# Performance work log

Hardware: AMD Instinct MI355X
Metric: run time of the kernel (lower is better)

The kernel has to match this reference:

```python
import jax, jax.numpy as jnp
import numpy as np

N_NODES = 50000
N_EDGES = 600000
D_OBJ = 128
D_REL = 128
D_OUT = 128


def setup_inputs() -> dict:
    key = jax.random.key(0)
    ks = jax.random.split(key, 7)
    s_obj = 1.0 / np.sqrt(D_OBJ)
    s_rel = 1.0 / np.sqrt(D_REL)
    return {
        "obj_vecs": jax.random.normal(ks[0], (N_NODES, D_OBJ), dtype=jnp.float32),
        "rel_vecs": jax.random.normal(ks[1], (N_EDGES, D_REL), dtype=jnp.float32),
        "edge_index": jax.random.randint(ks[2], (N_EDGES, 2), 0, N_NODES, dtype=jnp.int64),
        "W_obj": jax.random.normal(ks[3], (D_OUT, D_OBJ), dtype=jnp.float32) * s_obj,
        "b_obj": jax.random.normal(ks[4], (D_OUT,), dtype=jnp.float32) * s_obj,
        "W_rel": jax.random.normal(ks[5], (D_OUT, D_REL), dtype=jnp.float32) * s_rel,
        "b_rel": jax.random.normal(ks[6], (D_OUT,), dtype=jnp.float32) * s_rel,
    }


def reference(obj_vecs, rel_vecs, edge_index, W_obj, b_obj, W_rel, b_rel):
    # Per-node linear once ([N, d_out]) instead of twice per edge -- same math
    # since lin_obj(x_i) + lin_obj(x_j) = (x_i W^T + b) + (x_j W^T + b).
    obj_lin = obj_vecs @ W_obj.T + b_obj            # [N, d_out]
    rel_lin = rel_vecs @ W_rel.T + b_rel            # [E, d_out]
    src = edge_index[:, 0]
    dst = edge_index[:, 1]
    # message = relu(lin_obj(obj_i) + lin_rel(rel_k) + lin_obj(obj_j))
    msg = jax.nn.relu(obj_lin[src] + rel_lin + obj_lin[dst])  # [E, d_out]
    # aggr='add', flow source_to_target: scatter-add at target nodes (col 1)
    aggr = jax.ops.segment_sum(msg, dst, num_segments=obj_vecs.shape[0])
    return jax.nn.relu(aggr)
```

## Files before the change

kernel.cpp:

```cpp
#include <hip/hip_runtime.h>

#define N_NODES 50000
#define N_EDGES 600000
#define DD 128

typedef __attribute__((ext_vector_type(8))) short short8;
typedef __attribute__((ext_vector_type(4))) float f32x4;

__device__ __forceinline__ short f2bf(float f) {
    union { float f; unsigned u; } v; v.f = f;
    unsigned r = v.u + 0x7fffu + ((v.u >> 16) & 1u);
    return (short)(r >> 16);
}
__device__ __forceinline__ float bf2f(short s) {
    union { float f; unsigned u; } v; v.u = ((unsigned)(unsigned short)s) << 16;
    return v.f;
}
__device__ __forceinline__ float u2f(unsigned u) {
    union { float f; unsigned u; } v; v.u = u;
    return v.f;
}

__global__ __launch_bounds__(256) void k_lin(const float* __restrict__ X,
                                             const float* __restrict__ W,
                                             const float* __restrict__ bias,
                                             short* __restrict__ Y,
                                             int ntiles) {
    __shared__ __align__(16) short Wf[128 * 128];
    for (int i = threadIdx.x; i < 2048; i += 256) {
        const int fl = i & 63, fr = i >> 6;
        const int nt = fr >> 2, ks = fr & 3, fg = fl >> 4, fln = fl & 15;
        const float* s = W + (nt * 16 + fln) * DD + ks * 32 + fg * 8;
        short* d = Wf + i * 8;
#pragma unroll
        for (int j = 0; j < 8; ++j) d[j] = f2bf(s[j]);
    }
    __syncthreads();

    const int wave = threadIdx.x >> 6;
    const int lane = threadIdx.x & 63;
    const int g = lane >> 4, ln = lane & 15;

    float bb[8];
#pragma unroll
    for (int nt = 0; nt < 8; ++nt) bb[nt] = bias[nt * 16 + ln];

    for (int t = blockIdx.x * 4 + wave; t < ntiles; t += gridDim.x * 4) {
        const float* xr = X + (size_t)(t * 16 + ln) * DD;
        short8 a[4];
#pragma unroll
        for (int ks = 0; ks < 4; ++ks) {
            const float* p = xr + ks * 32 + g * 8;
            float4 t0 = *(const float4*)p;
            float4 t1 = *(const float4*)(p + 4);
            short8 v;
            v[0] = f2bf(t0.x); v[1] = f2bf(t0.y); v[2] = f2bf(t0.z); v[3] = f2bf(t0.w);
            v[4] = f2bf(t1.x); v[5] = f2bf(t1.y); v[6] = f2bf(t1.z); v[7] = f2bf(t1.w);
            a[ks] = v;
        }
#pragma unroll
        for (int nt = 0; nt < 8; ++nt) {
            f32x4 acc = {0.f, 0.f, 0.f, 0.f};
#pragma unroll
            for (int ks = 0; ks < 4; ++ks) {
                short8 b = *(const short8*)(Wf + (((nt << 2) + ks) * 64 + lane) * 8);
                acc = __builtin_amdgcn_mfma_f32_16x16x32_bf16(a[ks], b, acc, 0, 0, 0);
            }
#pragma unroll
            for (int r = 0; r < 4; ++r)
                Y[(size_t)(t * 16 + g * 4 + r) * DD + nt * 16 + ln] = f2bf(acc[r] + bb[nt]);
        }
    }
}

__global__ __launch_bounds__(256) void k_count(const int* __restrict__ EI,
                                               int* __restrict__ counts) {
    int e = blockIdx.x * 256 + threadIdx.x;
    if (e < N_EDGES) atomicAdd(&counts[EI[2 * e + 1]], 1);
}

__global__ __launch_bounds__(256) void k_scan1(const int* __restrict__ counts,
                                               int* __restrict__ scanned,
                                               int* __restrict__ bsum) {
    __shared__ int tmp[256];
    const int t = threadIdx.x;
    const int i = blockIdx.x * 256 + t;
    int v = (i < N_NODES) ? counts[i] : 0;
    tmp[t] = v;
    __syncthreads();
#pragma unroll
    for (int off = 1; off < 256; off <<= 1) {
        int x = (t >= off) ? tmp[t - off] : 0;
        __syncthreads();
        tmp[t] += x;
        __syncthreads();
    }
    if (i < N_NODES) scanned[i] = tmp[t] - v;
    if (t == 255) bsum[blockIdx.x] = tmp[255];
}

__global__ __launch_bounds__(256) void k_scan3m(const int* __restrict__ scanned,
                                                const int* __restrict__ bsum,
                                                int* __restrict__ offsets,
                                                int* __restrict__ cursor,
                                                int nb) {
    __shared__ int red[256];
    const int t = threadIdx.x;
    const int bid = blockIdx.x;
    red[t] = (t < bid && t < nb) ? bsum[t] : 0;
    __syncthreads();
#pragma unroll
    for (int off = 128; off > 0; off >>= 1) {
        if (t < off) red[t] += red[t + off];
        __syncthreads();
    }
    const int pre = red[0];
    const int i = bid * 256 + t;
    if (i < N_NODES) {
        const int off = scanned[i] + pre;
        offsets[i] = off;
        cursor[i] = off;
    }
    if (i == 0) offsets[N_NODES] = N_EDGES;
}

__global__ __launch_bounds__(256) void k_scatter2(const int* __restrict__ EI,
                                                  int* __restrict__ cursor,
                                                  int* __restrict__ perm) {
    int e = blockIdx.x * 256 + threadIdx.x;
    if (e < N_EDGES)
        perm[e] = atomicAdd(&cursor[EI[2 * e + 1]], 1);
}

__global__ __launch_bounds__(256) void k_fl(const float* __restrict__ RV,
                                            const int* __restrict__ EI,
                                            const int* __restrict__ perm,
                                            const float* __restrict__ W,
                                            const float* __restrict__ bias,
                                            const short* __restrict__ OL,
                                            unsigned* __restrict__ Ysw) {
    __shared__ __align__(16) short Wf[128 * 128];
    __shared__ __align__(16) unsigned stg[4][1160];

    for (int i = threadIdx.x; i < 2048; i += 256) {
        const int fl = i & 63, fr = i >> 6;
        const int nt = fr >> 2, ks = fr & 3, fg = fl >> 4, fln = fl & 15;
        const float* s = W + (nt * 16 + fln) * DD + ks * 32 + fg * 8;
        short* d = Wf + i * 8;
#pragma unroll
        for (int j = 0; j < 8; ++j) d[j] = f2bf(s[j]);
    }
    __syncthreads();

    const int wave = threadIdx.x >> 6;
    const int lane = threadIdx.x & 63;
    const int g = lane >> 4, ln = lane & 15;
    unsigned* st = stg[wave];

    const float br0 = bias[2 * lane];
    const float br1 = bias[2 * lane + 1];
    const unsigned short* OLu = (const unsigned short*)OL;
    const int NT = N_EDGES / 16;

    for (int t = blockIdx.x * 4 + wave; t < NT; t += gridDim.x * 4) {
        const int e0 = t * 16;

        const float* xr = RV + (size_t)(e0 + ln) * DD;
        short8 a[4];
#pragma unroll
        for (int ks = 0; ks < 4; ++ks) {
            const float* p = xr + ks * 32 + g * 8;
            float4 t0 = *(const float4*)p;
            float4 t1 = *(const float4*)(p + 4);
            short8 v;
            v[0] = f2bf(t0.x); v[1] = f2bf(t0.y); v[2] = f2bf(t0.z); v[3] = f2bf(t0.w);
            v[4] = f2bf(t1.x); v[5] = f2bf(t1.y); v[6] = f2bf(t1.z); v[7] = f2bf(t1.w);
            a[ks] = v;
        }

        int sp = 0, pp = 0;
        if (lane < 16) {
            sp = EI[2 * (e0 + lane)];
            pp = perm[e0 + lane];
        }

        f32x4 acc[8];
#pragma unroll
        for (int nt = 0; nt < 8; ++nt) {
            acc[nt] = (f32x4){0.f, 0.f, 0.f, 0.f};
#pragma unroll
            for (int ks = 0; ks < 4; ++ks) {
                short8 b = *(const short8*)(Wf + (((nt << 2) + ks) * 64 + lane) * 8);
                acc[nt] = __builtin_amdgcn_mfma_f32_16x16x32_bf16(a[ks], b, acc[nt], 0, 0, 0);
            }
        }

#pragma unroll
        for (int nt = 0; nt < 8; ++nt) {
            const unsigned lo = ((unsigned)(unsigned short)f2bf(acc[nt][0])) |
                                (((unsigned)(unsigned short)f2bf(acc[nt][1])) << 16);
            const unsigned hi = ((unsigned)(unsigned short)f2bf(acc[nt][2])) |
                                (((unsigned)(unsigned short)f2bf(acc[nt][3])) << 16);
            const int c = nt * 16 + ln;
            st[c * 9 + g * 2]     = lo;
            st[c * 9 + g * 2 + 1] = hi;
        }

#pragma unroll 8
        for (int e = 0; e < 16; ++e) {
            const int src = __shfl(sp, e);
            const int pos = __shfl(pp, e);
            const unsigned w0 = st[(2 * lane) * 9 + (e >> 1)];
            const unsigned w1 = st[(2 * lane + 1) * 9 + (e >> 1)];
            const float s0 = (e & 1) ? u2f(w0 & 0xffff0000u) : u2f(w0 << 16);
            const float s1 = (e & 1) ? u2f(w1 & 0xffff0000u) : u2f(w1 << 16);
            const unsigned olw = *(const unsigned*)(OLu + (size_t)src * DD + 2 * lane);
            const float y0 = s0 + br0 + u2f(olw << 16);
            const float y1 = s1 + br1 + u2f(olw & 0xffff0000u);
            const unsigned yw = ((unsigned)(unsigned short)f2bf(y0)) |
                                (((unsigned)(unsigned short)f2bf(y1)) << 16);
            Ysw[(size_t)pos * (DD / 2) + lane] = yw;
        }
    }
}

__global__ __launch_bounds__(256) void k_segsum(const unsigned* __restrict__ Ysw,
                                                const short* __restrict__ OL,
                                                const int* __restrict__ offs,
                                                float* __restrict__ out) {
    const int wave = threadIdx.x >> 6;
    const int lane = threadIdx.x & 63;
    const int v = blockIdx.x * 4 + wave;
    if (v >= N_NODES) return;

    const int r0 = offs[v], r1 = offs[v + 1];
    const unsigned short* OLu = (const unsigned short*)OL;
    const unsigned odw = *(const unsigned*)(OLu + (size_t)v * DD + 2 * lane);
    const float od0 = u2f(odw << 16), od1 = u2f(odw & 0xffff0000u);

    float a0 = 0.f, a1 = 0.f;
    int r = r0;
    for (; r + 4 <= r1; r += 4) {
        unsigned y[4];
#pragma unroll
        for (int j = 0; j < 4; ++j)
            y[j] = Ysw[(size_t)(r + j) * (DD / 2) + lane];
#pragma unroll
        for (int j = 0; j < 4; ++j) {
            a0 += fmaxf(u2f(y[j] << 16) + od0, 0.f);
            a1 += fmaxf(u2f(y[j] & 0xffff0000u) + od1, 0.f);
        }
    }
    for (; r < r1; ++r) {
        const unsigned yw = Ysw[(size_t)r * (DD / 2) + lane];
        a0 += fmaxf(u2f(yw << 16) + od0, 0.f);
        a1 += fmaxf(u2f(yw & 0xffff0000u) + od1, 0.f);
    }

    float2 o;
    o.x = fmaxf(a0, 0.f);
    o.y = fmaxf(a1, 0.f);
    *(float2*)(out + (size_t)v * DD + 2 * lane) = o;
}

extern "C" void kernel_launch(void* const* d_in, const int* in_sizes, int n_in,
                              void* d_out, int out_size, void* d_ws, size_t ws_size,
                              hipStream_t stream) {
    const float* obj = (const float*)d_in[0];
    const float* rel = (const float*)d_in[1];
    const int*   ei  = (const int*)d_in[2];
    const float* Wo  = (const float*)d_in[3];
    const float* bo  = (const float*)d_in[4];
    const float* Wr  = (const float*)d_in[5];
    const float* br  = (const float*)d_in[6];
    float* out = (float*)d_out;

    char* ws = (char*)d_ws;
    unsigned* Ysw  = (unsigned*)ws;
    short* OLb     = (short*)(ws + 153600000);
    int*   perm    = (int*)(ws + 166400000);
    int*   counts  = (int*)(ws + 168800000);
    int*   scanned = (int*)(ws + 169000192);
    int*   offsets = (int*)(ws + 169200896);
    int*   cursor  = (int*)(ws + 169401600);
    int*   bsum    = (int*)(ws + 169601792);

    const int NB_E = (N_EDGES + 255) / 256;
    const int NB_N = (N_NODES + 255) / 256;

    hipMemsetAsync(counts, 0, N_NODES * sizeof(int), stream);
    k_count<<<NB_E, 256, 0, stream>>>(ei, counts);
    k_scan1<<<NB_N, 256, 0, stream>>>(counts, scanned, bsum);
    k_scan3m<<<NB_N, 256, 0, stream>>>(scanned, bsum, offsets, cursor, NB_N);
    k_scatter2<<<NB_E, 256, 0, stream>>>(ei, cursor, perm);
    k_lin<<<782, 256, 0, stream>>>(obj, Wo, bo, OLb, N_NODES / 16);
    k_fl<<<2048, 256, 0, stream>>>(rel, ei, perm, Wr, br, OLb, Ysw);
    k_segsum<<<(N_NODES + 3) / 4, 256, 0, stream>>>(Ysw, OLb, offsets, out);
}
```

Baseline: 238.3 us.

## Use nontemporal input loads, transpose LDS staging, split segsum edges across half-waves

Input fp32 loads in the two GEMM kernels become nontemporal so the streamed activations do not evict reused data from cache. The k_fl staging buffer is re-laid out so each lane reads one word per edge pair, halving LDS reads in the scatter loop. k_segsum now lets each half-wave handle alternate edges with 8-byte loads and combines the halves with a cross-lane shuffle, which doubles memory-level parallelism per node. The price is an extra reduction step and idle lanes on the final store.

```diff
diff --git a/kernel.cpp b/kernel.cpp
--- a/kernel.cpp
+++ b/kernel.cpp
@@ -19,6 +19,10 @@
 __device__ __forceinline__ float u2f(unsigned u) {
     union { float f; unsigned u; } v; v.u = u;
     return v.f;
+}
+__device__ __forceinline__ unsigned packbf(float a, float b) {
+    return ((unsigned)(unsigned short)f2bf(a)) |
+           (((unsigned)(unsigned short)f2bf(b)) << 16);
 }
 
 __global__ __launch_bounds__(256) void k_lin(const float* __restrict__ X,
@@ -50,12 +54,12 @@
         short8 a[4];
 #pragma unroll
         for (int ks = 0; ks < 4; ++ks) {
-            const float* p = xr + ks * 32 + g * 8;
-            float4 t0 = *(const float4*)p;
-            float4 t1 = *(const float4*)(p + 4);
+            const f32x4* p = (const f32x4*)(xr + ks * 32 + g * 8);
+            const f32x4 t0 = __builtin_nontemporal_load(p);
+            const f32x4 t1 = __builtin_nontemporal_load(p + 1);
             short8 v;
-            v[0] = f2bf(t0.x); v[1] = f2bf(t0.y); v[2] = f2bf(t0.z); v[3] = f2bf(t0.w);
-            v[4] = f2bf(t1.x); v[5] = f2bf(t1.y); v[6] = f2bf(t1.z); v[7] = f2bf(t1.w);
+            v[0] = f2bf(t0[0]); v[1] = f2bf(t0[1]); v[2] = f2bf(t0[2]); v[3] = f2bf(t0[3]);
+            v[4] = f2bf(t1[0]); v[5] = f2bf(t1[1]); v[6] = f2bf(t1[2]); v[7] = f2bf(t1[3]);
             a[ks] = v;
         }
 #pragma unroll
@@ -140,7 +144,7 @@
                                             const short* __restrict__ OL,
                                             unsigned* __restrict__ Ysw) {
     __shared__ __align__(16) short Wf[128 * 128];
-    __shared__ __align__(16) unsigned stg[4][1160];
+    __shared__ __align__(16) unsigned stg[4][8 * 136];
 
     for (int i = threadIdx.x; i < 2048; i += 256) {
         const int fl = i & 63, fr = i >> 6;
@@ -169,12 +173,12 @@
         short8 a[4];
 #pragma unroll
         for (int ks = 0; ks < 4; ++ks) {
-            const float* p = xr + ks * 32 + g * 8;
-            float4 t0 = *(const float4*)p;
-            float4 t1 = *(const float4*)(p + 4);
+            const f32x4* p = (const f32x4*)(xr + ks * 32 + g * 8);
+            const f32x4 t0 = __builtin_nontemporal_load(p);
+            const f32x4 t1 = __builtin_nontemporal_load(p + 1);
             short8 v;
-            v[0] = f2bf(t0.x); v[1] = f2bf(t0.y); v[2] = f2bf(t0.z); v[3] = f2bf(t0.w);
-            v[4] = f2bf(t1.x); v[5] = f2bf(t1.y); v[6] = f2bf(t1.z); v[7] = f2bf(t1.w);
+            v[0] = f2bf(t0[0]); v[1] = f2bf(t0[1]); v[2] = f2bf(t0[2]); v[3] = f2bf(t0[3]);
+            v[4] = f2bf(t1[0]); v[5] = f2bf(t1[1]); v[6] = f2bf(t1[2]); v[7] = f2bf(t1[3]);
             a[ks] = v;
         }
 
@@ -197,29 +201,27 @@
 
 #pragma unroll
         for (int nt = 0; nt < 8; ++nt) {
-            const unsigned lo = ((unsigned)(unsigned short)f2bf(acc[nt][0])) |
-                                (((unsigned)(unsigned short)f2bf(acc[nt][1])) << 16);
-            const unsigned hi = ((unsigned)(unsigned short)f2bf(acc[nt][2])) |
-                                (((unsigned)(unsigned short)f2bf(acc[nt][3])) << 16);
             const int c = nt * 16 + ln;
-            st[c * 9 + g * 2]     = lo;
-            st[c * 9 + g * 2 + 1] = hi;
-        }
-
-#pragma unroll 8
-        for (int e = 0; e < 16; ++e) {
-            const int src = __shfl(sp, e);
-            const int pos = __shfl(pp, e);
-            const unsigned w0 = st[(2 * lane) * 9 + (e >> 1)];
-            const unsigned w1 = st[(2 * lane + 1) * 9 + (e >> 1)];
-            const float s0 = (e & 1) ? u2f(w0 & 0xffff0000u) : u2f(w0 << 16);
-            const float s1 = (e & 1) ? u2f(w1 & 0xffff0000u) : u2f(w1 << 16);
-            const unsigned olw = *(const unsigned*)(OLu + (size_t)src * DD + 2 * lane);
-            const float y0 = s0 + br0 + u2f(olw << 16);
-            const float y1 = s1 + br1 + u2f(olw & 0xffff0000u);
-            const unsigned yw = ((unsigned)(unsigned short)f2bf(y0)) |
-                                (((unsigned)(unsigned short)f2bf(y1)) << 16);
-            Ysw[(size_t)pos * (DD / 2) + lane] = yw;
+            st[(g * 2) * 136 + c]     = packbf(acc[nt][0], acc[nt][1]);
+            st[(g * 2 + 1) * 136 + c] = packbf(acc[nt][2], acc[nt][3]);
+        }
+
+#pragma unroll
+        for (int ep = 0; ep < 8; ++ep) {
+            const unsigned qx = st[ep * 136 + 2 * lane];
+            const unsigned qy = st[ep * 136 + 2 * lane + 1];
+#pragma unroll
+            for (int sub = 0; sub < 2; ++sub) {
+                const int e = 2 * ep + sub;
+                const int src = __shfl(sp, e);
+                const int pos = __shfl(pp, e);
+                const float s0 = sub ? u2f(qx & 0xffff0000u) : u2f(qx << 16);
+                const float s1 = sub ? u2f(qy & 0xffff0000u) : u2f(qy << 16);
+                const unsigned olw = *(const unsigned*)(OLu + (size_t)src * DD + 2 * lane);
+                const float y0 = s0 + br0 + u2f(olw << 16);
+                const float y1 = s1 + br1 + u2f(olw & 0xffff0000u);
+                Ysw[(size_t)pos * (DD / 2) + lane] = packbf(y0, y1);
+            }
         }
     }
 }
@@ -234,33 +236,33 @@
     if (v >= N_NODES) return;
 
     const int r0 = offs[v], r1 = offs[v + 1];
+    const int half = lane >> 5;
+    const int q = lane & 31;
     const unsigned short* OLu = (const unsigned short*)OL;
-    const unsigned odw = *(const unsigned*)(OLu + (size_t)v * DD + 2 * lane);
-    const float od0 = u2f(odw << 16), od1 = u2f(odw & 0xffff0000u);
-
-    float a0 = 0.f, a1 = 0.f;
-    int r = r0;
-    for (; r + 4 <= r1; r += 4) {
-        unsigned y[4];
-#pragma unroll
-        for (int j = 0; j < 4; ++j)
-            y[j] = Ysw[(size_t)(r + j) * (DD / 2) + lane];
-#pragma unroll
-        for (int j = 0; j < 4; ++j) {
-            a0 += fmaxf(u2f(y[j] << 16) + od0, 0.f);
-            a1 += fmaxf(u2f(y[j] & 0xffff0000u) + od1, 0.f);
-        }
-    }
-    for (; r < r1; ++r) {
-        const unsigned yw = Ysw[(size_t)r * (DD / 2) + lane];
-        a0 += fmaxf(u2f(yw << 16) + od0, 0.f);
-        a1 += fmaxf(u2f(yw & 0xffff0000u) + od1, 0.f);
-    }
-
-    float2 o;
-    o.x = fmaxf(a0, 0.f);
-    o.y = fmaxf(a1, 0.f);
-    *(float2*)(out + (size_t)v * DD + 2 * lane) = o;
+
+    const uint2 odw = *(const uint2*)(OLu + (size_t)v * DD + 4 * q);
+    const float od0 = u2f(odw.x << 16), od1 = u2f(odw.x & 0xffff0000u);
+    const float od2 = u2f(odw.y << 16), od3 = u2f(odw.y & 0xffff0000u);
+
+    float a0 = 0.f, a1 = 0.f, a2 = 0.f, a3 = 0.f;
+    for (int r = r0 + half; r < r1; r += 2) {
+        const uint2 y = *(const uint2*)(Ysw + (size_t)r * (DD / 2) + 2 * q);
+        a0 += fmaxf(u2f(y.x << 16) + od0, 0.f);
+        a1 += fmaxf(u2f(y.x & 0xffff0000u) + od1, 0.f);
+        a2 += fmaxf(u2f(y.y << 16) + od2, 0.f);
+        a3 += fmaxf(u2f(y.y & 0xffff0000u) + od3, 0.f);
+    }
+    a0 += __shfl_xor(a0, 32);
+    a1 += __shfl_xor(a1, 32);
+    a2 += __shfl_xor(a2, 32);
+    a3 += __shfl_xor(a3, 32);
+
+    if (half == 0) {
+        float4 o;
+        o.x = fmaxf(a0, 0.f); o.y = fmaxf(a1, 0.f);
+        o.z = fmaxf(a2, 0.f); o.w = fmaxf(a3, 0.f);
+        *(float4*)(out + (size_t)v * DD + 4 * q) = o;
+    }
 }
 
 extern "C" void kernel_launch(void* const* d_in, const int* in_sizes, int n_in,
```

Result: no change. 238.2 us (median of 2 runs) (-0.1%).
